# Performance work log

Hardware: AMD Instinct MI355X
Metric: run time of the kernel (lower is better)

Reference implementation:

```python
import jax, jax.numpy as jnp
import numpy as np

NEG_SLOPE = 0.01  # torch F.leaky_relu default


def setup_inputs() -> dict:
    key = jax.random.key(0)
    k1, k2, k3, k4 = jax.random.split(key, 4)
    B, N, F_in, F_out = 16, 2048, 128, 128
    stdv = 1.0 / np.sqrt(F_out)
    h = jax.random.normal(k1, (B, N, F_in), dtype=jnp.float32)
    adj = jax.random.uniform(k2, (B, N, N), dtype=jnp.float32)
    W = jax.random.uniform(k3, (F_in, F_out), minval=-stdv, maxval=stdv, dtype=jnp.float32)
    a = jax.random.uniform(k4, (2 * F_out, 1), minval=-stdv, maxval=stdv, dtype=jnp.float32)
    return {"h": h, "adj": adj, "W": W, "a": a}


def reference(h, adj, W, a):
    # Wh: [B, N, F_out]
    Wh = jnp.matmul(h, W)
    F_out = W.shape[1]
    a1 = a[:F_out, 0]  # [F_out]
    a2 = a[F_out:, 0]  # [F_out]
    # concat-score factorizes: e[b,i,j] = leaky(Wh[b,i]@a1 + Wh[b,j]@a2)
    f1 = jnp.einsum('bnf,f->bn', Wh, a1)  # [B, N]
    f2 = jnp.einsum('bnf,f->bn', Wh, a2)  # [B, N]
    e = jax.nn.leaky_relu(f1[:, :, None] + f2[:, None, :], negative_slope=NEG_SLOPE)  # [B,N,N]
    # NOTE: original softmax is over dim=1 (row index i), faithfully preserved
    attention = jax.nn.softmax(e, axis=1)
    h_prime = jnp.einsum('bij,bjf->bif', attention, Wh)  # bmm
    return h_prime
```

## Files before the change

### kernel.cpp

```cpp
#include <hip/hip_runtime.h>

#define BB 16
#define NN 2048
#define FF 128
#define NEG 0.01f
#define CH 32
#define CL (NN / CH)

__global__ __launch_bounds__(256) void k_wh(const float* __restrict__ h,
                                            const float* __restrict__ Wg,
                                            const float* __restrict__ a,
                                            float* __restrict__ Wh,
                                            float* __restrict__ f1,
                                            float* __restrict__ f2) {
    __shared__ float Ws[64 * 128];
    __shared__ float hsT[64 * 36];

    const int tid  = threadIdx.x;
    const int fg   = tid & 31;
    const int slot = tid >> 5;
    const int f4   = fg * 4;
    const int rowBase = blockIdx.x * 32;

    float acc[4][4];
#pragma unroll
    for (int r = 0; r < 4; ++r)
#pragma unroll
        for (int c = 0; c < 4; ++c) acc[r][c] = 0.f;

    const float4* Wg4 = (const float4*)Wg;
    const float4* hg4 = (const float4*)h;

    for (int kh = 0; kh < 128; kh += 64) {
        __syncthreads();
        for (int idx = tid; idx < 64 * 32; idx += 256) {
            int kk = idx >> 5, ff = idx & 31;
            ((float4*)Ws)[kk * 32 + ff] = Wg4[(size_t)(kh + kk) * 32 + ff];
        }
#pragma unroll
        for (int pass = 0; pass < 2; ++pass) {
            int idx = pass * 256 + tid;
            int kq = idx & 15, row = idx >> 4;
            float4 h4 = hg4[(size_t)(rowBase + row) * 32 + (kh >> 2) + kq];
            hsT[(kq * 4 + 0) * 36 + row] = h4.x;
            hsT[(kq * 4 + 1) * 36 + row] = h4.y;
            hsT[(kq * 4 + 2) * 36 + row] = h4.z;
            hsT[(kq * 4 + 3) * 36 + row] = h4.w;
        }
        __syncthreads();
#pragma unroll 8
        for (int kk = 0; kk < 64; ++kk) {
            float4 wv = *(const float4*)&Ws[kk * 128 + f4];
            float4 hv = *(const float4*)&hsT[kk * 36 + slot * 4];
            acc[0][0] += hv.x * wv.x; acc[0][1] += hv.x * wv.y; acc[0][2] += hv.x * wv.z; acc[0][3] += hv.x * wv.w;
            acc[1][0] += hv.y * wv.x; acc[1][1] += hv.y * wv.y; acc[1][2] += hv.y * wv.z; acc[1][3] += hv.y * wv.w;
            acc[2][0] += hv.z * wv.x; acc[2][1] += hv.z * wv.y; acc[2][2] += hv.z * wv.z; acc[2][3] += hv.z * wv.w;
            acc[3][0] += hv.w * wv.x; acc[3][1] += hv.w * wv.y; acc[3][2] += hv.w * wv.z; acc[3][3] += hv.w * wv.w;
        }
    }

    const float4* ag4 = (const float4*)a;
    float4 a1v = ag4[fg];
    float4 a2v = ag4[32 + fg];

#pragma unroll
    for (int r = 0; r < 4; ++r) {
        int row = rowBase + slot * 4 + r;
        float4 o; o.x = acc[r][0]; o.y = acc[r][1]; o.z = acc[r][2]; o.w = acc[r][3];
        *(float4*)&Wh[(size_t)row * 128 + f4] = o;
        float p1 = acc[r][0] * a1v.x + acc[r][1] * a1v.y + acc[r][2] * a1v.z + acc[r][3] * a1v.w;
        float p2 = acc[r][0] * a2v.x + acc[r][1] * a2v.y + acc[r][2] * a2v.z + acc[r][3] * a2v.w;
#pragma unroll
        for (int m = 16; m >= 1; m >>= 1) {
            p1 += __shfl_xor(p1, m);
            p2 += __shfl_xor(p2, m);
        }
        if (fg == 0) { f1[row] = p1; f2[row] = p2; }
    }
}

__device__ __forceinline__ float wave_incl_scan(float s, int lane) {
#pragma unroll
    for (int m = 1; m <= 32; m <<= 1) {
        float o = __shfl_up(s, m);
        if (lane >= m) s += o;
    }
    return s;
}

#define WAVE_SYNC() do { __builtin_amdgcn_wave_barrier(); asm volatile("" ::: "memory"); } while (0)

__global__ __launch_bounds__(1024) void k_sort2(const float* __restrict__ f1,
                                                const float* __restrict__ f2,
                                                float* __restrict__ SF1g,
                                                float* __restrict__ PAg,
                                                float* __restrict__ SAg,
                                                float* __restrict__ SKg,
                                                int* __restrict__ PERM,
                                                int* __restrict__ KIDX) {
    __shared__ float sKey[NN];
    __shared__ int   sIdx[NN];
    __shared__ float wtot[16];

    const int tid  = threadIdx.x;
    const int lane = tid & 63;
    const int w    = tid >> 6;
    const int b    = blockIdx.x & 15;
    const int task = blockIdx.x >> 4;

    const float* f1b = f1 + b * NN;
    const float* f2b = f2 + b * NN;

    if (task == 0) {
        for (int i = tid; i < NN; i += 1024) sKey[i] = f1b[i];
    } else {
        for (int i = tid; i < NN; i += 1024) { sKey[i] = f2b[i]; sIdx[i] = i; }
    }

    int prevj = 1024;
    for (int k = 2; k <= NN; k <<= 1) {
        for (int j = k >> 1; j > 0; j >>= 1) {
            if (j >= 128 || prevj >= 128) __syncthreads();
            else WAVE_SYNC();
            int mask = j - 1;
            int i   = ((tid & ~mask) << 1) | (tid & mask);
            int ixj = i | j;
            bool up = ((i & k) == 0);
            float av = sKey[i], bv = sKey[ixj];
            if ((av > bv) == up) {
                sKey[i] = bv; sKey[ixj] = av;
                if (task == 1) { int t2 = sIdx[i]; sIdx[i] = sIdx[ixj]; sIdx[ixj] = t2; }
            }
            prevj = j;
        }
    }
    __syncthreads();

    if (task == 0) {
        for (int i = tid; i < NN; i += 1024) SF1g[b * NN + i] = sKey[i];
        const size_t pbase = (size_t)b * (NN + 1);
        {
            float a0 = expf(NEG * sKey[2 * tid]);
            float a1 = expf(NEG * sKey[2 * tid + 1]);
            float s = a0 + a1;
            float v = wave_incl_scan(s, lane);
            if (lane == 63) wtot[w] = v;
            __syncthreads();
            float off = 0.f;
#pragma unroll
            for (int ww = 0; ww < 16; ++ww) off += (ww < w) ? wtot[ww] : 0.f;
            float excl = off + v - s;
            PAg[pbase + 2 * tid]     = excl;
            PAg[pbase + 2 * tid + 1] = excl + a0;
            if (tid == 1023) PAg[pbase + NN] = off + v;
        }
        __syncthreads();
        {
            float y0 = expf(sKey[NN - 1 - 2 * tid]);
            float y1 = expf(sKey[NN - 2 - 2 * tid]);
            float s = y0 + y1;
            float v = wave_incl_scan(s, lane);
            if (lane == 63) wtot[w] = v;
            __syncthreads();
            float off = 0.f;
#pragma unroll
            for (int ww = 0; ww < 16; ++ww) off += (ww < w) ? wtot[ww] : 0.f;
            SAg[pbase + NN - 1 - 2 * tid] = off + (v - s) + y0;
            SAg[pbase + NN - 2 - 2 * tid] = off + v;
            if (tid == 0) SAg[pbase + NN] = 0.f;
        }
    } else {
        for (int i = tid; i < NN; i += 1024) {
            SKg[b * NN + i]  = sKey[i];
            PERM[b * NN + i] = sIdx[i];
        }
        for (int i = tid; i < NN; i += 1024) {
            float tau = -f1b[i];
            int lo = 0, hi = NN;
            while (lo < hi) { int m = (lo + hi) >> 1; if (sKey[m] <= tau) lo = m + 1; else hi = m; }
            KIDX[b * NN + i] = lo;
        }
    }
}

__global__ __launch_bounds__(256) void k_uw(const float* __restrict__ SF1g,
                                            const float* __restrict__ PAg,
                                            const float* __restrict__ SAg,
                                            const float* __restrict__ SKg,
                                            float* __restrict__ Uarr,
                                            float* __restrict__ Warr) {
    __shared__ float sS[NN];
    __shared__ float sP[NN + 1];
    __shared__ float sA[NN + 1];
    const int b = blockIdx.x, tid = threadIdx.x;
    const size_t pbase = (size_t)b * (NN + 1);
    for (int i = tid; i < NN; i += 256) sS[i] = SF1g[b * NN + i];
    for (int i = tid; i < NN + 1; i += 256) { sP[i] = PAg[pbase + i]; sA[i] = SAg[pbase + i]; }
    __syncthreads();
    for (int t = tid; t < NN; t += 256) {
        float f2v = SKg[b * NN + t];
        float tau = -f2v;
        int lo = 0, hi = NN;
        while (lo < hi) { int m = (lo + hi) >> 1; if (sS[m] <= tau) lo = m + 1; else hi = m; }
        float eS = expf(NEG * f2v);
        float eF = expf(f2v);
        float inv = 1.0f / (eS * sP[lo] + eF * sA[lo]);
        Uarr[b * NN + t] = eF * inv;
        Warr[b * NN + t] = eS * inv;
    }
}

__global__ __launch_bounds__(128) void k_chunk(const float* __restrict__ Wh,
                                               const float* __restrict__ Uarr,
                                               const float* __restrict__ Warr,
                                               const int* __restrict__ PERM,
                                               float* __restrict__ CU,
                                               float* __restrict__ CW) {
    int blk = blockIdx.x;
    int b = blk / CH, c = blk % CH;
    int f = threadIdx.x;
    int base = b * NN + c * CL;
    const float* Whb = Wh + (size_t)b * NN * FF;
    float aU = 0.f, aW = 0.f;
#pragma unroll 4
    for (int t = 0; t < CL; ++t) {
        int j = PERM[base + t];
        float uv = Uarr[base + t], wv = Warr[base + t];
        float whv = Whb[(size_t)j * FF + f];
        aU += uv * whv; aW += wv * whv;
    }
    CU[(size_t)blk * 128 + f] = aU;
    CW[(size_t)blk * 128 + f] = aW;
}

__global__ __launch_bounds__(128) void k_offsets(float* __restrict__ CU,
                                                 float* __restrict__ CW) {
    int b = blockIdx.x, f = threadIdx.x;
    float aU = 0.f, aW = 0.f;
#pragma unroll
    for (int c = 0; c < CH; ++c) {
        size_t idx = (size_t)(b * CH + c) * 128 + f;
        float tU = CU[idx], tW = CW[idx];
        CU[idx] = aU; CW[idx] = aW;
        aU += tU; aW += tW;
    }
}

__global__ __launch_bounds__(128) void k_prefix(const float* __restrict__ Wh,
                                                const float* __restrict__ Uarr,
                                                const float* __restrict__ Warr,
                                                const int* __restrict__ PERM,
                                                const float* __restrict__ CU,
                                                const float* __restrict__ CW,
                                                float* __restrict__ PU,
                                                float* __restrict__ PW) {
    int blk = blockIdx.x;
    int b = blk / CH, c = blk % CH;
    int f = threadIdx.x;
    int base = b * NN + c * CL;
    const float* Whb = Wh + (size_t)b * NN * FF;
    float aU = CU[(size_t)blk * 128 + f];
    float aW = CW[(size_t)blk * 128 + f];
    size_t rowB = (size_t)b * (NN + 1);
#pragma unroll 4
    for (int t = 0; t < CL; ++t) {
        int g = c * CL + t;
        PU[(rowB + g) * FF + f] = aU;
        PW[(rowB + g) * FF + f] = aW;
        int j = PERM[base + t];
        float whv = Whb[(size_t)j * FF + f];
        aU += Uarr[base + t] * whv;
        aW += Warr[base + t] * whv;
    }
    if (c == CH - 1) {
        PU[(rowB + NN) * FF + f] = aU;
        PW[(rowB + NN) * FF + f] = aW;
    }
}

__global__ __launch_bounds__(256) void k_out(const float* __restrict__ PU,
                                             const float* __restrict__ PW,
                                             const float* __restrict__ f1,
                                             const int* __restrict__ KIDX,
                                             float* __restrict__ out) {
    int rowId = blockIdx.x * 2 + (threadIdx.x >> 7);
    int f = threadIdx.x & 127;
    int b = rowId >> 11;
    int k = KIDX[rowId];
    float f1v = f1[rowId];
    float alpha = expf(NEG * f1v);
    float beta  = expf(f1v);
    size_t rowB = (size_t)b * (NN + 1);
    float totU = PU[(rowB + NN) * FF + f];
    float pu   = PU[(rowB + k) * FF + f];
    float pw   = PW[(rowB + k) * FF + f];
    out[(size_t)rowId * FF + f] = alpha * pw + beta * (totU - pu);
}

extern "C" void kernel_launch(void* const* d_in, const int* in_sizes, int n_in,
                              void* d_out, int out_size, void* d_ws, size_t ws_size,
                              hipStream_t stream) {
    const float* h  = (const float*)d_in[0];
    const float* W  = (const float*)d_in[2];
    const float* a  = (const float*)d_in[3];
    float* out = (float*)d_out;

    float* ws = (float*)d_ws;
    float* Wh   = ws;  ws += (size_t)BB * NN * FF;
    float* f1   = ws;  ws += BB * NN;
    float* f2   = ws;  ws += BB * NN;
    float* SF1  = ws;  ws += BB * NN;
    float* PA   = ws;  ws += BB * (NN + 1);
    float* SA   = ws;  ws += BB * (NN + 1);
    float* SK   = ws;  ws += BB * NN;
    float* Uarr = ws;  ws += BB * NN;
    float* Warr = ws;  ws += BB * NN;
    float* CU   = ws;  ws += BB * CH * FF;
    float* CW   = ws;  ws += BB * CH * FF;
    float* PU   = ws;  ws += (size_t)BB * (NN + 1) * FF;
    float* PW   = ws;  ws += (size_t)BB * (NN + 1) * FF;
    int* PERM = (int*)ws;  ws += BB * NN;
    int* KIDX = (int*)ws;

    k_wh     <<<(BB * NN) / 32, 256, 0, stream>>>(h, W, a, Wh, f1, f2);
    k_sort2  <<<2 * BB, 1024, 0, stream>>>(f1, f2, SF1, PA, SA, SK, PERM, KIDX);
    k_uw     <<<BB, 256, 0, stream>>>(SF1, PA, SA, SK, Uarr, Warr);
    k_chunk  <<<BB * CH, 128, 0, stream>>>(Wh, Uarr, Warr, PERM, CU, CW);
    k_offsets<<<BB, 128, 0, stream>>>(CU, CW);
    k_prefix <<<BB * CH, 128, 0, stream>>>(Wh, Uarr, Warr, PERM, CU, CW, PU, PW);
    k_out    <<<(BB * NN) / 2, 256, 0, stream>>>(PU, PW, f1, KIDX, out);
}
```

Before: 390.9 us.

## Fuse U/W, chunk sums, offsets and prefix into one decoupled-lookback scan kernel

Replaces four kernels (k_uw, k_chunk, k_offsets, k_prefix) with a single k_scan that computes each chunk's U/W weights locally and reads the gathered Wh rows only once, caching the products in shared memory. Chunk offsets are resolved through a decoupled look-back scan using flags and atomics, which removes the second gather pass over Wh and three kernel launches. In exchange it relies on inter-block spin-waiting, which needs forward progress of earlier blocks, and adds a memset of the flag array. The k_uw work is also spread over 512 blocks instead of 16.

```diff
diff --git a/kernel.cpp b/kernel.cpp
--- a/kernel.cpp
+++ b/kernel.cpp
@@ -183,98 +183,119 @@
     }
 }
 
-__global__ __launch_bounds__(256) void k_uw(const float* __restrict__ SF1g,
-                                            const float* __restrict__ PAg,
-                                            const float* __restrict__ SAg,
-                                            const float* __restrict__ SKg,
-                                            float* __restrict__ Uarr,
-                                            float* __restrict__ Warr) {
-    __shared__ float sS[NN];
-    __shared__ float sP[NN + 1];
-    __shared__ float sA[NN + 1];
-    const int b = blockIdx.x, tid = threadIdx.x;
+__global__ __launch_bounds__(256) void k_scan(const float* __restrict__ Wh,
+                                              const float* __restrict__ SF1g,
+                                              const float* __restrict__ PAg,
+                                              const float* __restrict__ SAg,
+                                              const float* __restrict__ SKg,
+                                              const int* __restrict__ PERM,
+                                              float* __restrict__ AGGU,
+                                              float* __restrict__ AGGW,
+                                              float* __restrict__ INCU,
+                                              float* __restrict__ INCW,
+                                              int* __restrict__ FLAG,
+                                              float* __restrict__ PU,
+                                              float* __restrict__ PW) {
+    __shared__ float sSF1[NN];
+    __shared__ float prodU[CL][FF];
+    __shared__ float prodW[CL][FF];
+    __shared__ float sU[CL], sW[CL];
+    __shared__ int   sJ[CL];
+    __shared__ float redU[2][FF], redW[2][FF];
+
+    const int blk  = blockIdx.x;
+    const int b    = blk / CH, c = blk % CH;
+    const int tid  = threadIdx.x;
+    const int f    = tid & 127;
+    const int half = tid >> 7;
+    const int base = b * NN + c * CL;
     const size_t pbase = (size_t)b * (NN + 1);
-    for (int i = tid; i < NN; i += 256) sS[i] = SF1g[b * NN + i];
-    for (int i = tid; i < NN + 1; i += 256) { sP[i] = PAg[pbase + i]; sA[i] = SAg[pbase + i]; }
+
+    for (int i = tid; i < NN; i += 256) sSF1[i] = SF1g[b * NN + i];
+    if (tid >= 64 && tid < 64 + CL) sJ[tid - 64] = PERM[base + tid - 64];
     __syncthreads();
-    for (int t = tid; t < NN; t += 256) {
-        float f2v = SKg[b * NN + t];
+
+    if (tid < CL) {
+        int t = tid;
+        float f2v = SKg[base + t];
         float tau = -f2v;
         int lo = 0, hi = NN;
-        while (lo < hi) { int m = (lo + hi) >> 1; if (sS[m] <= tau) lo = m + 1; else hi = m; }
+        while (lo < hi) { int m = (lo + hi) >> 1; if (sSF1[m] <= tau) lo = m + 1; else hi = m; }
         float eS = expf(NEG * f2v);
         float eF = expf(f2v);
-        float inv = 1.0f / (eS * sP[lo] + eF * sA[lo]);
-        Uarr[b * NN + t] = eF * inv;
-        Warr[b * NN + t] = eS * inv;
-    }
-}
-
-__global__ __launch_bounds__(128) void k_chunk(const float* __restrict__ Wh,
-                                               const float* __restrict__ Uarr,
-                                               const float* __restrict__ Warr,
-                                               const int* __restrict__ PERM,
-                                               float* __restrict__ CU,
-                                               float* __restrict__ CW) {
-    int blk = blockIdx.x;
-    int b = blk / CH, c = blk % CH;
-    int f = threadIdx.x;
-    int base = b * NN + c * CL;
+        float inv = 1.0f / (eS * PAg[pbase + lo] + eF * SAg[pbase + lo]);
+        sU[t] = eF * inv;
+        sW[t] = eS * inv;
+    }
+    __syncthreads();
+
     const float* Whb = Wh + (size_t)b * NN * FF;
-    float aU = 0.f, aW = 0.f;
+    float tU = 0.f, tW = 0.f;
 #pragma unroll 4
-    for (int t = 0; t < CL; ++t) {
-        int j = PERM[base + t];
-        float uv = Uarr[base + t], wv = Warr[base + t];
-        float whv = Whb[(size_t)j * FF + f];
-        aU += uv * whv; aW += wv * whv;
-    }
-    CU[(size_t)blk * 128 + f] = aU;
-    CW[(size_t)blk * 128 + f] = aW;
-}
-
-__global__ __launch_bounds__(128) void k_offsets(float* __restrict__ CU,
-                                                 float* __restrict__ CW) {
-    int b = blockIdx.x, f = threadIdx.x;
-    float aU = 0.f, aW = 0.f;
-#pragma unroll
-    for (int c = 0; c < CH; ++c) {
-        size_t idx = (size_t)(b * CH + c) * 128 + f;
-        float tU = CU[idx], tW = CW[idx];
-        CU[idx] = aU; CW[idx] = aW;
-        aU += tU; aW += tW;
-    }
-}
-
-__global__ __launch_bounds__(128) void k_prefix(const float* __restrict__ Wh,
-                                                const float* __restrict__ Uarr,
-                                                const float* __restrict__ Warr,
-                                                const int* __restrict__ PERM,
-                                                const float* __restrict__ CU,
-                                                const float* __restrict__ CW,
-                                                float* __restrict__ PU,
-                                                float* __restrict__ PW) {
-    int blk = blockIdx.x;
-    int b = blk / CH, c = blk % CH;
-    int f = threadIdx.x;
-    int base = b * NN + c * CL;
-    const float* Whb = Wh + (size_t)b * NN * FF;
-    float aU = CU[(size_t)blk * 128 + f];
-    float aW = CW[(size_t)blk * 128 + f];
-    size_t rowB = (size_t)b * (NN + 1);
+    for (int tt = 0; tt < CL / 2; ++tt) {
+        int t = tt * 2 + half;
+        float whv = Whb[(size_t)sJ[t] * FF + f];
+        float pu = sU[t] * whv, pw = sW[t] * whv;
+        prodU[t][f] = pu; prodW[t][f] = pw;
+        tU += pu; tW += pw;
+    }
+    redU[half][f] = tU; redW[half][f] = tW;
+    __syncthreads();
+    float totU = redU[0][f] + redU[1][f];
+    float totW = redW[0][f] + redW[1][f];
+
+    if (c == 0) {
+        if (half == 0) __hip_atomic_store(&INCU[(size_t)blk * FF + f], totU, __ATOMIC_RELAXED, __HIP_MEMORY_SCOPE_AGENT);
+        else           __hip_atomic_store(&INCW[(size_t)blk * FF + f], totW, __ATOMIC_RELAXED, __HIP_MEMORY_SCOPE_AGENT);
+        __syncthreads();
+        if (tid == 0) { __threadfence(); __hip_atomic_store(&FLAG[blk], 2, __ATOMIC_RELEASE, __HIP_MEMORY_SCOPE_AGENT); }
+    } else {
+        if (half == 0) __hip_atomic_store(&AGGU[(size_t)blk * FF + f], totU, __ATOMIC_RELAXED, __HIP_MEMORY_SCOPE_AGENT);
+        else           __hip_atomic_store(&AGGW[(size_t)blk * FF + f], totW, __ATOMIC_RELAXED, __HIP_MEMORY_SCOPE_AGENT);
+        __syncthreads();
+        if (tid == 0) { __threadfence(); __hip_atomic_store(&FLAG[blk], 1, __ATOMIC_RELEASE, __HIP_MEMORY_SCOPE_AGENT); }
+    }
+
+    float offU = 0.f, offW = 0.f;
+    if (c != 0) {
+        int p = blk - 1;
+        while (true) {
+            int fl;
+            do { fl = __hip_atomic_load(&FLAG[p], __ATOMIC_ACQUIRE, __HIP_MEMORY_SCOPE_AGENT); } while (fl == 0);
+            if (fl == 2) {
+                offU += __hip_atomic_load(&INCU[(size_t)p * FF + f], __ATOMIC_RELAXED, __HIP_MEMORY_SCOPE_AGENT);
+                offW += __hip_atomic_load(&INCW[(size_t)p * FF + f], __ATOMIC_RELAXED, __HIP_MEMORY_SCOPE_AGENT);
+                break;
+            } else {
+                offU += __hip_atomic_load(&AGGU[(size_t)p * FF + f], __ATOMIC_RELAXED, __HIP_MEMORY_SCOPE_AGENT);
+                offW += __hip_atomic_load(&AGGW[(size_t)p * FF + f], __ATOMIC_RELAXED, __HIP_MEMORY_SCOPE_AGENT);
+                p--;
+            }
+        }
+        if (half == 0) __hip_atomic_store(&INCU[(size_t)blk * FF + f], offU + totU, __ATOMIC_RELAXED, __HIP_MEMORY_SCOPE_AGENT);
+        else           __hip_atomic_store(&INCW[(size_t)blk * FF + f], offW + totW, __ATOMIC_RELAXED, __HIP_MEMORY_SCOPE_AGENT);
+        __syncthreads();
+        if (tid == 0) { __threadfence(); __hip_atomic_store(&FLAG[blk], 2, __ATOMIC_RELEASE, __HIP_MEMORY_SCOPE_AGENT); }
+    }
+
+    if (half == 0) {
+        float aU = offU;
 #pragma unroll 4
-    for (int t = 0; t < CL; ++t) {
-        int g = c * CL + t;
-        PU[(rowB + g) * FF + f] = aU;
-        PW[(rowB + g) * FF + f] = aW;
-        int j = PERM[base + t];
-        float whv = Whb[(size_t)j * FF + f];
-        aU += Uarr[base + t] * whv;
-        aW += Warr[base + t] * whv;
-    }
-    if (c == CH - 1) {
-        PU[(rowB + NN) * FF + f] = aU;
-        PW[(rowB + NN) * FF + f] = aW;
+        for (int t = 0; t < CL; ++t) {
+            int g = c * CL + t;
+            PU[(pbase + g) * FF + f] = aU;
+            aU += prodU[t][f];
+        }
+        if (c == CH - 1) PU[(pbase + NN) * FF + f] = aU;
+    } else {
+        float aW = offW;
+#pragma unroll 4
+        for (int t = 0; t < CL; ++t) {
+            int g = c * CL + t;
+            PW[(pbase + g) * FF + f] = aW;
+            aW += prodW[t][f];
+        }
+        if (c == CH - 1) PW[(pbase + NN) * FF + f] = aW;
     }
 }
 
@@ -313,20 +334,20 @@
     float* PA   = ws;  ws += BB * (NN + 1);
     float* SA   = ws;  ws += BB * (NN + 1);
     float* SK   = ws;  ws += BB * NN;
-    float* Uarr = ws;  ws += BB * NN;
-    float* Warr = ws;  ws += BB * NN;
-    float* CU   = ws;  ws += BB * CH * FF;
-    float* CW   = ws;  ws += BB * CH * FF;
+    float* AGGU = ws;  ws += BB * CH * FF;
+    float* AGGW = ws;  ws += BB * CH * FF;
+    float* INCU = ws;  ws += BB * CH * FF;
+    float* INCW = ws;  ws += BB * CH * FF;
     float* PU   = ws;  ws += (size_t)BB * (NN + 1) * FF;
     float* PW   = ws;  ws += (size_t)BB * (NN + 1) * FF;
     int* PERM = (int*)ws;  ws += BB * NN;
-    int* KIDX = (int*)ws;
-
-    k_wh     <<<(BB * NN) / 32, 256, 0, stream>>>(h, W, a, Wh, f1, f2);
-    k_sort2  <<<2 * BB, 1024, 0, stream>>>(f1, f2, SF1, PA, SA, SK, PERM, KIDX);
-    k_uw     <<<BB, 256, 0, stream>>>(SF1, PA, SA, SK, Uarr, Warr);
-    k_chunk  <<<BB * CH, 128, 0, stream>>>(Wh, Uarr, Warr, PERM, CU, CW);
-    k_offsets<<<BB, 128, 0, stream>>>(CU, CW);
-    k_prefix <<<BB * CH, 128, 0, stream>>>(Wh, Uarr, Warr, PERM, CU, CW, PU, PW);
-    k_out    <<<(BB * NN) / 2, 256, 0, stream>>>(PU, PW, f1, KIDX, out);
-}
+    int* KIDX = (int*)ws;  ws += BB * NN;
+    int* FLAG = (int*)ws;
+
+    hipMemsetAsync(FLAG, 0, BB * CH * sizeof(int), stream);
+    k_wh   <<<(BB * NN) / 32, 256, 0, stream>>>(h, W, a, Wh, f1, f2);
+    k_sort2<<<2 * BB, 1024, 0, stream>>>(f1, f2, SF1, PA, SA, SK, PERM, KIDX);
+    k_scan <<<BB * CH, 256, 0, stream>>>(Wh, SF1, PA, SA, SK, PERM,
+                                         AGGU, AGGW, INCU, INCW, FLAG, PU, PW);
+    k_out  <<<(BB * NN) / 2, 256, 0, stream>>>(PU, PW, f1, KIDX, out);
+}
```

Result: slower. 553.4 us (+41.6%).

## Fuse prefix-sum materialization into output kernel, eliminating PU/PW buffers

Applied to the files above, without the earlier changes.

Removes the full per-row prefix arrays PU/PW (about 2x16x2049x128 floats written, then gathered) by having each chunk block find the output rows whose threshold index falls inside its chunk. It walks those rows in sorted-f1 order, advances the running prefix in registers from a shared-memory copy of the chunk's Wh rows, and writes the outputs directly. It also fuses the U/W computation into the chunk-sum kernel and precomputes the threshold indices in sorted order, which cuts two launches. The cost is serial per-block work that depends on how rows are distributed across chunks, so load may be imbalanced, plus an extra sort permutation.

```diff
diff --git a/kernel.cpp b/kernel.cpp
--- a/kernel.cpp
+++ b/kernel.cpp
@@ -93,10 +93,11 @@
 __global__ __launch_bounds__(1024) void k_sort2(const float* __restrict__ f1,
                                                 const float* __restrict__ f2,
                                                 float* __restrict__ SF1g,
+                                                int* __restrict__ PERM1,
                                                 float* __restrict__ PAg,
                                                 float* __restrict__ SAg,
                                                 float* __restrict__ SKg,
-                                                int* __restrict__ PERM,
+                                                int* __restrict__ PERM2,
                                                 int* __restrict__ KIDX) {
     __shared__ float sKey[NN];
     __shared__ int   sIdx[NN];
@@ -110,12 +111,9 @@
 
     const float* f1b = f1 + b * NN;
     const float* f2b = f2 + b * NN;
-
-    if (task == 0) {
-        for (int i = tid; i < NN; i += 1024) sKey[i] = f1b[i];
-    } else {
-        for (int i = tid; i < NN; i += 1024) { sKey[i] = f2b[i]; sIdx[i] = i; }
-    }
+    const float* src = (task == 0) ? f1b : f2b;
+
+    for (int i = tid; i < NN; i += 1024) { sKey[i] = src[i]; sIdx[i] = i; }
 
     int prevj = 1024;
     for (int k = 2; k <= NN; k <<= 1) {
@@ -129,7 +127,7 @@
             float av = sKey[i], bv = sKey[ixj];
             if ((av > bv) == up) {
                 sKey[i] = bv; sKey[ixj] = av;
-                if (task == 1) { int t2 = sIdx[i]; sIdx[i] = sIdx[ixj]; sIdx[ixj] = t2; }
+                int t2 = sIdx[i]; sIdx[i] = sIdx[ixj]; sIdx[ixj] = t2;
             }
             prevj = j;
         }
@@ -137,7 +135,10 @@
     __syncthreads();
 
     if (task == 0) {
-        for (int i = tid; i < NN; i += 1024) SF1g[b * NN + i] = sKey[i];
+        for (int i = tid; i < NN; i += 1024) {
+            SF1g[b * NN + i]  = sKey[i];
+            PERM1[b * NN + i] = sIdx[i];
+        }
         const size_t pbase = (size_t)b * (NN + 1);
         {
             float a0 = expf(NEG * sKey[2 * tid]);
@@ -171,8 +172,8 @@
         }
     } else {
         for (int i = tid; i < NN; i += 1024) {
-            SKg[b * NN + i]  = sKey[i];
-            PERM[b * NN + i] = sIdx[i];
+            SKg[b * NN + i]   = sKey[i];
+            PERM2[b * NN + i] = sIdx[i];
         }
         for (int i = tid; i < NN; i += 1024) {
             float tau = -f1b[i];
@@ -183,118 +184,144 @@
     }
 }
 
-__global__ __launch_bounds__(256) void k_uw(const float* __restrict__ SF1g,
-                                            const float* __restrict__ PAg,
-                                            const float* __restrict__ SAg,
-                                            const float* __restrict__ SKg,
-                                            float* __restrict__ Uarr,
-                                            float* __restrict__ Warr) {
-    __shared__ float sS[NN];
-    __shared__ float sP[NN + 1];
-    __shared__ float sA[NN + 1];
-    const int b = blockIdx.x, tid = threadIdx.x;
+__global__ __launch_bounds__(128) void k_uwchunk(const float* __restrict__ Wh,
+                                                 const float* __restrict__ SF1g,
+                                                 const float* __restrict__ PAg,
+                                                 const float* __restrict__ SAg,
+                                                 const float* __restrict__ SKg,
+                                                 const int* __restrict__ PERM2,
+                                                 float* __restrict__ Uarr,
+                                                 float* __restrict__ Warr,
+                                                 float* __restrict__ CU,
+                                                 float* __restrict__ CW) {
+    __shared__ float sSF1[NN];
+    __shared__ float sU[CL], sW[CL];
+    __shared__ int   sJ[CL];
+    const int blk = blockIdx.x;
+    const int b = blk / CH, c = blk % CH;
+    const int f = threadIdx.x;
+    const int base = b * NN + c * CL;
     const size_t pbase = (size_t)b * (NN + 1);
-    for (int i = tid; i < NN; i += 256) sS[i] = SF1g[b * NN + i];
-    for (int i = tid; i < NN + 1; i += 256) { sP[i] = PAg[pbase + i]; sA[i] = SAg[pbase + i]; }
+
+    for (int i = f; i < NN; i += 128) sSF1[i] = SF1g[b * NN + i];
+    if (f < CL) sJ[f] = PERM2[base + f];
     __syncthreads();
-    for (int t = tid; t < NN; t += 256) {
-        float f2v = SKg[b * NN + t];
+
+    if (f < CL) {
+        float f2v = SKg[base + f];
         float tau = -f2v;
         int lo = 0, hi = NN;
-        while (lo < hi) { int m = (lo + hi) >> 1; if (sS[m] <= tau) lo = m + 1; else hi = m; }
+        while (lo < hi) { int m = (lo + hi) >> 1; if (sSF1[m] <= tau) lo = m + 1; else hi = m; }
         float eS = expf(NEG * f2v);
         float eF = expf(f2v);
-        float inv = 1.0f / (eS * sP[lo] + eF * sA[lo]);
-        Uarr[b * NN + t] = eF * inv;
-        Warr[b * NN + t] = eS * inv;
-    }
-}
-
-__global__ __launch_bounds__(128) void k_chunk(const float* __restrict__ Wh,
-                                               const float* __restrict__ Uarr,
-                                               const float* __restrict__ Warr,
-                                               const int* __restrict__ PERM,
-                                               float* __restrict__ CU,
-                                               float* __restrict__ CW) {
-    int blk = blockIdx.x;
-    int b = blk / CH, c = blk % CH;
-    int f = threadIdx.x;
-    int base = b * NN + c * CL;
+        float inv = 1.0f / (eS * PAg[pbase + lo] + eF * SAg[pbase + lo]);
+        float u = eF * inv, wv = eS * inv;
+        sU[f] = u; sW[f] = wv;
+        Uarr[base + f] = u; Warr[base + f] = wv;
+    }
+    __syncthreads();
+
     const float* Whb = Wh + (size_t)b * NN * FF;
     float aU = 0.f, aW = 0.f;
-#pragma unroll 4
+#pragma unroll 8
     for (int t = 0; t < CL; ++t) {
-        int j = PERM[base + t];
-        float uv = Uarr[base + t], wv = Warr[base + t];
-        float whv = Whb[(size_t)j * FF + f];
-        aU += uv * whv; aW += wv * whv;
-    }
-    CU[(size_t)blk * 128 + f] = aU;
-    CW[(size_t)blk * 128 + f] = aW;
+        float whv = Whb[(size_t)sJ[t] * FF + f];
+        aU += sU[t] * whv;
+        aW += sW[t] * whv;
+    }
+    CU[(size_t)blk * FF + f] = aU;
+    CW[(size_t)blk * FF + f] = aW;
 }
 
 __global__ __launch_bounds__(128) void k_offsets(float* __restrict__ CU,
-                                                 float* __restrict__ CW) {
-    int b = blockIdx.x, f = threadIdx.x;
+                                                 float* __restrict__ CW,
+                                                 float* __restrict__ TOTU,
+                                                 const int* __restrict__ KIDX,
+                                                 const int* __restrict__ PERM1,
+                                                 int* __restrict__ KS) {
+    const int b = blockIdx.x, f = threadIdx.x;
     float aU = 0.f, aW = 0.f;
 #pragma unroll
     for (int c = 0; c < CH; ++c) {
-        size_t idx = (size_t)(b * CH + c) * 128 + f;
+        size_t idx = (size_t)(b * CH + c) * FF + f;
         float tU = CU[idx], tW = CW[idx];
         CU[idx] = aU; CW[idx] = aW;
         aU += tU; aW += tW;
     }
-}
-
-__global__ __launch_bounds__(128) void k_prefix(const float* __restrict__ Wh,
-                                                const float* __restrict__ Uarr,
-                                                const float* __restrict__ Warr,
-                                                const int* __restrict__ PERM,
-                                                const float* __restrict__ CU,
-                                                const float* __restrict__ CW,
-                                                float* __restrict__ PU,
-                                                float* __restrict__ PW) {
-    int blk = blockIdx.x;
-    int b = blk / CH, c = blk % CH;
-    int f = threadIdx.x;
-    int base = b * NN + c * CL;
+    TOTU[b * FF + f] = aU;
+    for (int pos = f; pos < NN; pos += 128)
+        KS[b * NN + pos] = KIDX[b * NN + PERM1[b * NN + pos]];
+}
+
+__global__ __launch_bounds__(128) void k_outfused(const float* __restrict__ Wh,
+                                                  const float* __restrict__ Uarr,
+                                                  const float* __restrict__ Warr,
+                                                  const int* __restrict__ PERM2,
+                                                  const float* __restrict__ CU,
+                                                  const float* __restrict__ CW,
+                                                  const float* __restrict__ TOTU,
+                                                  const int* __restrict__ KS,
+                                                  const int* __restrict__ PERM1,
+                                                  const float* __restrict__ SF1g,
+                                                  float* __restrict__ out) {
+    __shared__ float whv[CL][FF];
+    __shared__ float sU[CL], sW[CL];
+    __shared__ int   sJ[CL];
+    __shared__ int   sP[128];
+    __shared__ float sF[128];
+    __shared__ int   sK[128];
+
+    const int blk = blockIdx.x;
+    const int b = blk / CH, c = blk % CH;
+    const int f = threadIdx.x;
+    const int base = b * NN + c * CL;
+    const int* KSb = KS + b * NN;
+    const int lowv = CL * c;
+    const int upper = (c == CH - 1) ? (NN + 1) : CL * (c + 1);
+
+    int lo = 0, hi = NN;
+    while (lo < hi) { int m = (lo + hi) >> 1; if (KSb[m] < upper) hi = m; else lo = m + 1; }
+    const int segLo = lo;
+    lo = 0; hi = NN;
+    while (lo < hi) { int m = (lo + hi) >> 1; if (KSb[m] < lowv) hi = m; else lo = m + 1; }
+    const int segHi = lo;
+
+    if (f < CL) {
+        sU[f] = Uarr[base + f];
+        sW[f] = Warr[base + f];
+        sJ[f] = PERM2[base + f];
+    }
+    __syncthreads();
+
     const float* Whb = Wh + (size_t)b * NN * FF;
-    float aU = CU[(size_t)blk * 128 + f];
-    float aW = CW[(size_t)blk * 128 + f];
-    size_t rowB = (size_t)b * (NN + 1);
-#pragma unroll 4
-    for (int t = 0; t < CL; ++t) {
-        int g = c * CL + t;
-        PU[(rowB + g) * FF + f] = aU;
-        PW[(rowB + g) * FF + f] = aW;
-        int j = PERM[base + t];
-        float whv = Whb[(size_t)j * FF + f];
-        aU += Uarr[base + t] * whv;
-        aW += Warr[base + t] * whv;
-    }
-    if (c == CH - 1) {
-        PU[(rowB + NN) * FF + f] = aU;
-        PW[(rowB + NN) * FF + f] = aW;
-    }
-}
-
-__global__ __launch_bounds__(256) void k_out(const float* __restrict__ PU,
-                                             const float* __restrict__ PW,
-                                             const float* __restrict__ f1,
-                                             const int* __restrict__ KIDX,
-                                             float* __restrict__ out) {
-    int rowId = blockIdx.x * 2 + (threadIdx.x >> 7);
-    int f = threadIdx.x & 127;
-    int b = rowId >> 11;
-    int k = KIDX[rowId];
-    float f1v = f1[rowId];
-    float alpha = expf(NEG * f1v);
-    float beta  = expf(f1v);
-    size_t rowB = (size_t)b * (NN + 1);
-    float totU = PU[(rowB + NN) * FF + f];
-    float pu   = PU[(rowB + k) * FF + f];
-    float pw   = PW[(rowB + k) * FF + f];
-    out[(size_t)rowId * FF + f] = alpha * pw + beta * (totU - pu);
+#pragma unroll 8
+    for (int t = 0; t < CL; ++t) whv[t][f] = Whb[(size_t)sJ[t] * FF + f];
+
+    float aU = CU[(size_t)blk * FF + f];
+    float aW = CW[(size_t)blk * FF + f];
+    const float totU = TOTU[b * FF + f];
+    float* outb = out + (size_t)b * NN * FF;
+
+    int t = 0;
+    for (int start = segHi; start > segLo; ) {
+        int cnt = start - segLo; if (cnt > 128) cnt = 128;
+        int s0 = start - cnt;
+        __syncthreads();
+        if (f < cnt) {
+            int p = s0 + f;
+            sP[f] = PERM1[b * NN + p];
+            sF[f] = SF1g[b * NN + p];
+            sK[f] = KSb[p];
+        }
+        __syncthreads();
+        for (int q = cnt - 1; q >= 0; --q) {
+            int r = sK[q] - lowv;
+            while (t < r) { aU += sU[t] * whv[t][f]; aW += sW[t] * whv[t][f]; ++t; }
+            float f1v = sF[q];
+            outb[(size_t)sP[q] * FF + f] = expf(NEG * f1v) * aW + expf(f1v) * (totU - aU);
+        }
+        start = s0;
+    }
 }
 
 extern "C" void kernel_launch(void* const* d_in, const int* in_sizes, int n_in,
@@ -317,16 +344,15 @@
     float* Warr = ws;  ws += BB * NN;
     float* CU   = ws;  ws += BB * CH * FF;
     float* CW   = ws;  ws += BB * CH * FF;
-    float* PU   = ws;  ws += (size_t)BB * (NN + 1) * FF;
-    float* PW   = ws;  ws += (size_t)BB * (NN + 1) * FF;
-    int* PERM = (int*)ws;  ws += BB * NN;
-    int* KIDX = (int*)ws;
-
-    k_wh     <<<(BB * NN) / 32, 256, 0, stream>>>(h, W, a, Wh, f1, f2);
-    k_sort2  <<<2 * BB, 1024, 0, stream>>>(f1, f2, SF1, PA, SA, SK, PERM, KIDX);
-    k_uw     <<<BB, 256, 0, stream>>>(SF1, PA, SA, SK, Uarr, Warr);
-    k_chunk  <<<BB * CH, 128, 0, stream>>>(Wh, Uarr, Warr, PERM, CU, CW);
-    k_offsets<<<BB, 128, 0, stream>>>(CU, CW);
-    k_prefix <<<BB * CH, 128, 0, stream>>>(Wh, Uarr, Warr, PERM, CU, CW, PU, PW);
-    k_out    <<<(BB * NN) / 2, 256, 0, stream>>>(PU, PW, f1, KIDX, out);
-}
+    float* TOTU = ws;  ws += BB * FF;
+    int* PERM1 = (int*)ws;  ws += BB * NN;
+    int* PERM2 = (int*)ws;  ws += BB * NN;
+    int* KIDX  = (int*)ws;  ws += BB * NN;
+    int* KS    = (int*)ws;
+
+    k_wh      <<<(BB * NN) / 32, 256, 0, stream>>>(h, W, a, Wh, f1, f2);
+    k_sort2   <<<2 * BB, 1024, 0, stream>>>(f1, f2, SF1, PERM1, PA, SA, SK, PERM2, KIDX);
+    k_uwchunk <<<BB * CH, 128, 0, stream>>>(Wh, SF1, PA, SA, SK, PERM2, Uarr, Warr, CU, CW);
+    k_offsets <<<BB, 128, 0, stream>>>(CU, CW, TOTU, KIDX, PERM1, KS);
+    k_outfused<<<BB * CH, 128, 0, stream>>>(Wh, Uarr, Warr, PERM2, CU, CW, TOTU, KS, PERM1, SF1, out);
+}
```

Result: slower. 402.2 us (+2.9%).
